# Kernel tuning notes

Hardware: AMD Instinct MI355X
Metric: run time of the kernel (lower is better)

## Reference

```python
import jax, jax.numpy as jnp
import numpy as np

IN_CHANNELS = 512
NUM_HEADS = 8
PARTIAL = 4
PC = IN_CHANNELS // PARTIAL  # 128, per-branch dim


def _mha(x, wqkv, bqkv, wproj, bproj, num_heads):
    # Standard ViT-style attention block: fused qkv -> SDPA -> out proj.
    B, N, C = x.shape
    d = C // num_heads
    qkv = (x @ wqkv + bqkv).reshape(B, N, 3, num_heads, d)
    q, k, v = jnp.moveaxis(qkv, 2, 0)            # each (B, N, h, d)
    q = q.transpose(0, 2, 1, 3)                  # (B, h, N, d)
    k = k.transpose(0, 2, 1, 3)
    v = v.transpose(0, 2, 1, 3)
    scale = jnp.asarray(d, x.dtype) ** -0.5
    attn = jax.nn.softmax(jnp.einsum('bhqd,bhkd->bhqk', q, k) * scale, axis=-1)
    out = jnp.einsum('bhqk,bhkd->bhqd', attn, v)
    out = out.transpose(0, 2, 1, 3).reshape(B, N, C)
    return out @ wproj + bproj


def _channel_shuffle(x, groups):
    # ShuffleNet channel shuffle on (b, c, n, t)
    b, c, n, t = x.shape
    return x.reshape(b, groups, c // groups, n, t).transpose(0, 2, 1, 3, 4).reshape(b, c, n, t)


def setup_inputs() -> dict:
    key = jax.random.key(0)
    ks = jax.random.split(key, 13)
    b, n, t = 8, 25, 64
    inp = {'x': jax.random.normal(ks[0], (b, n, t, IN_CHANNELS), dtype=jnp.float32)}
    i = 1
    for name in ('t', 's', 'st'):
        inp[f'{name}_wqkv'] = jax.random.normal(ks[i], (PC, 3 * PC), dtype=jnp.float32) * 0.02; i += 1
        inp[f'{name}_bqkv'] = jnp.zeros((3 * PC,), dtype=jnp.float32)
        inp[f'{name}_wproj'] = jax.random.normal(ks[i], (PC, PC), dtype=jnp.float32) * 0.02; i += 1
        inp[f'{name}_bproj'] = jnp.zeros((PC,), dtype=jnp.float32)
    return inp


def reference(x, t_wqkv, t_bqkv, t_wproj, t_bproj,
              s_wqkv, s_bqkv, s_wproj, s_bproj,
              st_wqkv, st_bqkv, st_wproj, st_bproj):
    b, n, t, c = x.shape
    pc = PC
    # split order in forward: x_id, x_st, x_s, x_t (all width pc here)
    x_id = x[..., 0 * pc:1 * pc]
    x_st = x[..., 1 * pc:2 * pc]
    x_s = x[..., 2 * pc:3 * pc]
    x_t = x[..., 3 * pc:4 * pc]

    t_x = x_t.reshape(b * n, t, pc)                       # temporal: attend over t
    s_x = x_s.transpose(0, 2, 1, 3).reshape(b * t, n, pc)  # spatial: attend over n
    st_x = x_st.reshape(b, n * t, pc)                      # spatiotemporal: attend over n*t

    t_x = _mha(t_x, t_wqkv, t_bqkv, t_wproj, t_bproj, NUM_HEADS).reshape(b, n, t, pc)
    s_x = _mha(s_x, s_wqkv, s_bqkv, s_wproj, s_bproj, NUM_HEADS).reshape(b, t, n, pc).transpose(0, 2, 1, 3)
    st_x = _mha(st_x, st_wqkv, st_bqkv, st_wproj, st_bproj, NUM_HEADS).reshape(b, n, t, pc)

    # concat order: id, t, s, st (differs from split order), then to channels-first
    out = jnp.concatenate((x_id, t_x, s_x, st_x), axis=3).transpose(0, 3, 1, 2)  # (b, c, n, t)
    return _channel_shuffle(out, PARTIAL)
```

## Files before the change

kernel.cpp:

```cpp
#include <hip/hip_runtime.h>
#include <hip/hip_bf16.h>

#define BUF   1638400ull
#define QSC   0.36067376f

typedef __attribute__((ext_vector_type(4))) float f4;
typedef __attribute__((ext_vector_type(8))) short s8v;
typedef __attribute__((ext_vector_type(4))) unsigned u4v;

#if __has_builtin(__builtin_amdgcn_exp2f)
#define EXP2(x) __builtin_amdgcn_exp2f(x)
#else
#define EXP2(x) exp2f(x)
#endif

__device__ __forceinline__ short f2bf(float f) {
    __hip_bfloat16 h = __float2bfloat16(f);
    short s; __builtin_memcpy(&s, &h, 2); return s;
}
__device__ __forceinline__ unsigned pack2(float a, float b) {
    return (unsigned)(unsigned short)f2bf(a) | ((unsigned)(unsigned short)f2bf(b) << 16);
}
__device__ __forceinline__ float bf2f(short s) {
    return __uint_as_float((unsigned)(unsigned short)s << 16);
}
__device__ __forceinline__ unsigned tpack(float hi, float lo) {
    return __builtin_amdgcn_perm(__float_as_uint(hi), __float_as_uint(lo), 0x07060302u);
}

__global__ __launch_bounds__(256) void prep(
    const float* __restrict__ x,
    const float* __restrict__ wq0, const float* __restrict__ wq1,
    const float* __restrict__ wq2,
    const float* __restrict__ wp0, const float* __restrict__ wp1,
    const float* __restrict__ wp2,
    short* __restrict__ xbf, short* __restrict__ wsw)
{
    const int blk = blockIdx.x, tid = threadIdx.x;
    if (blk < 3200) {
        const int base = blk * 2048 + tid * 8;
        float4 a = *(const float4*)(x + base);
        float4 b = *(const float4*)(x + base + 4);
        s8v o;
        o[0]=f2bf(a.x); o[1]=f2bf(a.y); o[2]=f2bf(a.z); o[3]=f2bf(a.w);
        o[4]=f2bf(b.x); o[5]=f2bf(b.y); o[6]=f2bf(b.z); o[7]=f2bf(b.w);
        *(s8v*)(xbf + base) = o;
    } else {
        const int idx0 = (blk - 3200) * 2048 + tid * 8;
        const float* W; int Ncols, loc = idx0;
        if      (idx0 < 49152)  { W = wq0; Ncols = 384; }
        else if (idx0 < 98304)  { W = wq1; Ncols = 384; loc -= 49152; }
        else if (idx0 < 147456) { W = wq2; Ncols = 384; loc -= 98304; }
        else if (idx0 < 163840) { W = wp0; Ncols = 128; loc -= 147456; }
        else if (idx0 < 180224) { W = wp1; Ncols = 128; loc -= 163840; }
        else                    { W = wp2; Ncols = 128; loc -= 180224; }
        const int lane = (loc >> 3) & 63, ks = (loc >> 9) & 3, nt = loc >> 11;
        const int col = nt * 16 + (lane & 15);
        const int k0  = ks * 32 + 8 * (lane >> 4);
        s8v o;
#pragma unroll
        for (int j = 0; j < 8; j++) o[j] = f2bf(W[(k0 + j) * Ncols + col]);
        *(s8v*)(wsw + idx0) = o;
    }
}

__global__ __launch_bounds__(256) void qkv_all(
    const short* __restrict__ xbf, const short* __restrict__ wsw,
    const float* __restrict__ bq0, const float* __restrict__ bq1,
    const float* __restrict__ bq2,
    short* __restrict__ q0, short* __restrict__ k0, short* __restrict__ vt0,
    short* __restrict__ q1, short* __restrict__ k1, short* __restrict__ vt1,
    short* __restrict__ q2, short* __restrict__ k2, short* __restrict__ vt2)
{
    const int br = blockIdx.x / 800, tile = blockIdx.x % 800;
    const int tok0 = tile * 16;
    const int wave = threadIdx.x >> 6, lane = threadIdx.x & 63;
    const int c = lane & 15, gq = lane >> 4;
    const int off = 384 - 128 * br;
    const short* wswb = wsw + br * 49152;
    const float* bias = (br == 0) ? bq0 : (br == 1) ? bq1 : bq2;

    const short* xrow = xbf + (size_t)(tok0 + c) * 512 + off + 8 * gq;
    s8v af[4];
#pragma unroll
    for (int ks = 0; ks < 4; ks++) af[ks] = *(const s8v*)(xrow + ks * 32);

    const int batch0 = tok0 >> 6;
    const int b_  = tok0 / 1600;
    const int rm0 = tok0 - b_ * 1600;
    const int seq1 = rm0 >> 6;

    for (int nti = 0; nti < 6; nti++) {
        const int nt = wave * 6 + nti;
        const short* bp = wswb + ((size_t)(nt * 4) * 64 + lane) * 8;
        f4 acc = {0.f, 0.f, 0.f, 0.f};
#pragma unroll
        for (int ks = 0; ks < 4; ks++) {
            s8v bf = *(const s8v*)(bp + ks * 512);
            acc = __builtin_amdgcn_mfma_f32_16x16x32_bf16(af[ks], bf, acc, 0, 0, 0);
        }
        const float bv = bias[nt * 16 + c];
        const float v0 = acc[0]+bv, v1 = acc[1]+bv, v2 = acc[2]+bv, v3 = acc[3]+bv;
        const int which = nt >> 3, h = nt & 7;

        if (br == 0) {
            const int seq0 = (tok0 & 63) + 4 * gq;
            if (which == 2) {
                unsigned* p = (unsigned*)(vt0 + ((size_t)(batch0*8+h)*16 + c)*64 + seq0);
                p[0] = pack2(v0, v1); p[1] = pack2(v2, v3);
            } else {
                short* p = (which ? k0 : q0) + (((size_t)(batch0*8+h)*64 + seq0)*16 + c);
                p[0]=f2bf(v0); p[16]=f2bf(v1); p[32]=f2bf(v2); p[48]=f2bf(v3);
            }
        } else if (br == 1) {
            const int bt0 = b_ * 64 + (rm0 & 63) + 4 * gq;
            if (which == 2) {
                short* p = vt1 + ((size_t)(bt0*8+h)*16 + c)*25 + seq1;
                p[0]=f2bf(v0); p[3200]=f2bf(v1); p[6400]=f2bf(v2); p[9600]=f2bf(v3);
            } else {
                short* p = (which ? k1 : q1) + (((size_t)bt0*8+h)*25 + seq1)*16 + c;
                p[0]=f2bf(v0); p[3200]=f2bf(v1); p[6400]=f2bf(v2); p[9600]=f2bf(v3);
            }
        } else {
            const int seq0 = rm0 + 4 * gq;
            if (which == 2) {
                unsigned* p = (unsigned*)(vt2 + ((size_t)b_*128 + h*16 + c)*1600 + seq0);
                p[0] = pack2(v0, v1); p[1] = pack2(v2, v3);
            } else {
                short* p = (which ? k2 : q2) + (((size_t)b_*8+h)*1600 + seq0)*16 + c;
                p[0]=f2bf(v0); p[16]=f2bf(v1); p[32]=f2bf(v2); p[48]=f2bf(v3);
            }
        }
    }
}

template<int CHK, int NCH, bool KM>
__device__ __forceinline__ void attn_core(
    const short* __restrict__ qg, const short* __restrict__ kg,
    const short* __restrict__ vtg, const int vstride, const int nreal,
    short* kl, short* vt, const int stid, const int snum,
    const int lane, const int qt0, const int nq,
    float* __restrict__ obase, const int ostride)
{
    const int c = lane & 15, gq = lane >> 4;
    const int VS = CHK + 8;

    u4v qu = {0u, 0u, 0u, 0u};
    if (gq < 2) {
        const int qrow = KM ? min(qt0 + c, nq - 1) : (qt0 + c);
        const short* qr = qg + (size_t)qrow * 16 + 8 * gq;
        s8v raw = *(const s8v*)qr;
#pragma unroll
        for (int jp = 0; jp < 4; jp++)
            qu[jp] = tpack(bf2f(raw[2*jp+1]) * QSC, bf2f(raw[2*jp]) * QSC);
    }
    const s8v qf = __builtin_bit_cast(s8v, qu);

    s8v ones;
#pragma unroll
    for (int j = 0; j < 8; j++) ones[j] = (short)0x3F80;

    f4 oacc = {0.f,0.f,0.f,0.f}, lacc = {0.f,0.f,0.f,0.f};
    const int krow_base = 8 * (c >> 2) + (c & 3);

    for (int ch = 0; ch < NCH; ch++) {
        const int kb0 = ch * CHK;
        __syncthreads();
        if (KM) {
            for (int i = stid; i < CHK * 16 + 8; i += snum)
                kl[i] = (i < nreal * 16) ? kg[i] : (short)0;
            for (int i = stid; i < 16 * VS; i += snum) {
                int d = i / VS, col = i % VS;
                vt[i] = (col < nreal) ? vtg[(size_t)d * vstride + col] : (short)0;
            }
        } else {
            const unsigned* kgd = (const unsigned*)(kg + (size_t)kb0 * 16);
            unsigned* kld = (unsigned*)kl;
            for (int i = stid; i < CHK * 8 + 4; i += snum)
                kld[i] = (i < CHK * 8) ? kgd[i] : 0u;
            for (int i = stid; i < 16 * (CHK / 2); i += snum) {
                int d = i / (CHK / 2), cc = i % (CHK / 2);
                *(unsigned*)(vt + d * VS + 2 * cc) =
                    *(const unsigned*)(vtg + (size_t)d * vstride + kb0 + 2 * cc);
            }
        }
        __syncthreads();

#pragma unroll
        for (int st = 0; st < CHK / 32; st++) {
            const int kr0 = st * 32 + krow_base;
            s8v kf0 = *(const s8v*)(gq < 2 ? kl + kr0 * 16 + 8 * gq       : kl + CHK * 16);
            s8v kf1 = *(const s8v*)(gq < 2 ? kl + (kr0 + 4) * 16 + 8 * gq : kl + CHK * 16);
            s8v vf  = *(const s8v*)(vt + c * VS + st * 32 + 8 * gq);

            const f4 z = {0.f,0.f,0.f,0.f};
            f4 sa = __builtin_amdgcn_mfma_f32_16x16x32_bf16(kf0, qf, z, 0, 0, 0);
            f4 sb = __builtin_amdgcn_mfma_f32_16x16x32_bf16(kf1, qf, z, 0, 0, 0);

            float pa[4], pb[4];
#pragma unroll
            for (int r = 0; r < 4; r++) { pa[r] = EXP2(sa[r]); pb[r] = EXP2(sb[r]); }
            if (KM) {
#pragma unroll
                for (int r = 0; r < 4; r++) {
                    if (kb0 + st*32 + 8*gq + r     >= nreal) pa[r] = 0.f;
                    if (kb0 + st*32 + 8*gq + 4 + r >= nreal) pb[r] = 0.f;
                }
            }
            u4v pu;
            pu[0] = tpack(pa[1], pa[0]); pu[1] = tpack(pa[3], pa[2]);
            pu[2] = tpack(pb[1], pb[0]); pu[3] = tpack(pb[3], pb[2]);
            s8v pf = __builtin_bit_cast(s8v, pu);

            oacc = __builtin_amdgcn_mfma_f32_16x16x32_bf16(pf, vf,   oacc, 0, 0, 0);
            lacc = __builtin_amdgcn_mfma_f32_16x16x32_bf16(pf, ones, lacc, 0, 0, 0);
        }
    }

#pragma unroll
    for (int r = 0; r < 4; r++) {
        const int qrow = qt0 + 4 * gq + r;
        if (!KM || qrow < nq)
            obase[(size_t)qrow * ostride] = oacc[r] / lacc[r];
    }
}

__global__ __launch_bounds__(256) void attn_all(
    const short* __restrict__ q0, const short* __restrict__ k0, const short* __restrict__ vt0,
    const short* __restrict__ q1, const short* __restrict__ k1, const short* __restrict__ vt1,
    const short* __restrict__ q2, const short* __restrict__ k2, const short* __restrict__ vt2,
    float* __restrict__ ob0, float* __restrict__ ob1, float* __restrict__ ob2)
{
    __shared__ short smem[5264];
    const int blk = blockIdx.x, tid = threadIdx.x;
    const int wave = tid >> 6, lane = tid & 63;
    const int c = lane & 15;

    if (blk < 1600) {
        const int bh = blk / 25, b25 = blk % 25;
        const int qt0 = b25 * 64 + wave * 16;
        float* obase = ob2 + (size_t)(bh >> 3) * 1600 * 128 + (bh & 7) * 16 + c;
        attn_core<160, 10, false>(q2 + (size_t)bh * 25600, k2 + (size_t)bh * 25600,
                                  vt2 + (size_t)bh * 25600, 1600, 1600,
                                  smem, smem + 2568, tid, 256,
                                  lane, qt0, 1600, obase, 128);
    } else if (blk < 3200) {
        const int bh = blk - 1600;
        float* obase = ob0 + (size_t)(bh >> 3) * 64 * 128 + (bh & 7) * 16 + c;
        attn_core<64, 1, false>(q0 + (size_t)bh * 1024, k0 + (size_t)bh * 1024,
                                vt0 + (size_t)bh * 1024, 64, 64,
                                smem, smem + 1040, tid, 256,
                                lane, wave * 16, 64, obase, 128);
    } else {
        const int bs = blk - 3200;
        const int half = wave >> 1;
        const int bh = bs * 2 + half;
        const int qt0 = (wave & 1) * 16;
        short* kl = smem + half * 1160;
        const int bat = bh >> 3, h = bh & 7;
        const int b2 = bat >> 6, t2 = bat & 63;
        float* obase = ob1 + ((size_t)b2 * 1600 + t2) * 128 + h * 16 + c;
        attn_core<32, 1, true>(q1 + (size_t)bh * 400, k1 + (size_t)bh * 400,
                               vt1 + (size_t)bh * 400, 25, 25,
                               kl, kl + 520, tid & 127, 128,
                               lane, qt0, 25, obase, 8192);
    }
}

__global__ __launch_bounds__(256) void projid(
    const float* __restrict__ ob0, const float* __restrict__ ob1,
    const float* __restrict__ ob2, const short* __restrict__ wsw,
    const float* __restrict__ bp0, const float* __restrict__ bp1,
    const float* __restrict__ bp2,
    const float* __restrict__ x, float* __restrict__ out)
{
    __shared__ unsigned short xl[64 * 130];
    const int blk = blockIdx.x, tid = threadIdx.x;

    if (blk < 2400) {
        const int br = blk / 800, t8 = blk % 800;
        const float* obb = (br == 0) ? ob0 : (br == 1) ? ob1 : ob2;
        const float* bp  = (br == 0) ? bp0 : (br == 1) ? bp1 : bp2;
        const short* wswb = wsw + 147456 + br * 16384;
        const int grp = br + 1;
        const int tok0 = t8 * 16;
        const int wave = tid >> 6, lane = tid & 63;
        const int c = lane & 15, gq = lane >> 4;

        const float* arow = obb + (size_t)(tok0 + c) * 128 + 8 * gq;
        s8v af[4];
#pragma unroll
        for (int ks = 0; ks < 4; ks++) {
            float4 a = *(const float4*)(arow + ks * 32);
            float4 b = *(const float4*)(arow + ks * 32 + 4);
            af[ks][0]=f2bf(a.x); af[ks][1]=f2bf(a.y); af[ks][2]=f2bf(a.z); af[ks][3]=f2bf(a.w);
            af[ks][4]=f2bf(b.x); af[ks][5]=f2bf(b.y); af[ks][6]=f2bf(b.z); af[ks][7]=f2bf(b.w);
        }

        const int bn = t8 >> 2, b_ = bn / 25, n_ = bn % 25;
        const int t0 = (t8 & 3) * 16 + 4 * gq;

        for (int nti = 0; nti < 2; nti++) {
            const int nt = wave * 2 + nti;
            const short* bpw = wswb + ((size_t)(nt * 4) * 64 + lane) * 8;
            f4 acc = {0.f, 0.f, 0.f, 0.f};
#pragma unroll
            for (int ks = 0; ks < 4; ks++) {
                s8v bf = *(const s8v*)(bpw + ks * 512);
                acc = __builtin_amdgcn_mfma_f32_16x16x32_bf16(af[ks], bf, acc, 0, 0, 0);
            }
            const int c2 = nt * 16 + c;
            const float bv = bp[c2];
            float4 st = {acc[0]+bv, acc[1]+bv, acc[2]+bv, acc[3]+bv};
            *(float4*)(out + (size_t)b_ * 819200 + (size_t)(c2 * 4 + grp) * 1600
                           + n_ * 64 + t0) = st;
        }
    } else {
        const int bn = blk - 2400;
        const int b_ = bn / 25, n_ = bn % 25;
        for (int idx = tid; idx < 8192; idx += 256) {
            int row = idx >> 7, c2 = idx & 127;
            xl[row * 130 + c2] =
                (unsigned short)(__float_as_uint(x[(size_t)(bn * 64 + row) * 512 + c2]) >> 16);
        }
        __syncthreads();
        const int t_ = tid & 63, cg = tid >> 6;
        const size_t base = (size_t)b_ * 819200 + (size_t)n_ * 64 + t_;
#pragma unroll
        for (int i = 0; i < 32; i++) {
            int c2 = cg + 4 * i;
            out[base + (size_t)(c2 * 4 + 0) * 1600] =
                __uint_as_float((unsigned)xl[t_ * 130 + c2] << 16);
        }
    }
}

extern "C" void kernel_launch(void* const* d_in, const int* in_sizes, int n_in,
                              void* d_out, int out_size, void* d_ws, size_t ws_size,
                              hipStream_t stream)
{
    const float* x        = (const float*)d_in[0];
    const float* t_wqkv   = (const float*)d_in[1];
    const float* t_bqkv   = (const float*)d_in[2];
    const float* t_wproj  = (const float*)d_in[3];
    const float* t_bproj  = (const float*)d_in[4];
    const float* s_wqkv   = (const float*)d_in[5];
    const float* s_bqkv   = (const float*)d_in[6];
    const float* s_wproj  = (const float*)d_in[7];
    const float* s_bproj  = (const float*)d_in[8];
    const float* st_wqkv  = (const float*)d_in[9];
    const float* st_bqkv  = (const float*)d_in[10];
    const float* st_wproj = (const float*)d_in[11];
    const float* st_bproj = (const float*)d_in[12];

    short* xbf = (short*)d_ws;
    short* wsw = xbf + 6553600ull;
    short* qkv = wsw + 196608ull;
    short *q0 = qkv,           *k0 = qkv + BUF,     *vt0 = qkv + 2*BUF;
    short *q1 = qkv + 3*BUF,   *k1 = qkv + 4*BUF,   *vt1 = qkv + 5*BUF;
    short *q2 = qkv + 6*BUF,   *k2 = qkv + 7*BUF,   *vt2 = qkv + 8*BUF;
    float* ob0 = (float*)(qkv + 9*BUF);
    float* ob1 = ob0 + BUF;
    float* ob2 = ob0 + 2*BUF;
    float* out = (float*)d_out;

    prep<<<3296, 256, 0, stream>>>(x, t_wqkv, s_wqkv, st_wqkv,
                                   t_wproj, s_wproj, st_wproj, xbf, wsw);
    qkv_all<<<2400, 256, 0, stream>>>(xbf, wsw, t_bqkv, s_bqkv, st_bqkv,
                                      q0, k0, vt0, q1, k1, vt1, q2, k2, vt2);
    attn_all<<<5248, 256, 0, stream>>>(q0, k0, vt0, q1, k1, vt1, q2, k2, vt2,
                                       ob0, ob1, ob2);
    projid<<<2600, 256, 0, stream>>>(ob0, ob1, ob2, wsw,
                                     t_bproj, s_bproj, st_bproj, x, out);
}
```

Before: 189.1 us.

## Fuse temporal and spatial attention branches into single kernels keeping QKV in LDS

Splits the work by branch. The temporal and spatial branches each get one fused kernel that computes QKV, attention and the output projection with intermediates kept in shared memory, so their q/k/v and fp32 attention outputs no longer round-trip through global memory. The spatiotemporal branch keeps separate qkv, attention and projection kernels, but its attention output is now stored as bf16 instead of fp32. In exchange there are more kernel launches, and the fused kernels launch few blocks (200 and 512), which risks poor occupancy and serialization across the CUs.

```diff
diff --git a/kernel.cpp b/kernel.cpp
--- a/kernel.cpp
+++ b/kernel.cpp
@@ -26,6 +26,12 @@
 }
 __device__ __forceinline__ unsigned tpack(float hi, float lo) {
     return __builtin_amdgcn_perm(__float_as_uint(hi), __float_as_uint(lo), 0x07060302u);
+}
+__device__ __forceinline__ s8v ones_frag() {
+    s8v o;
+#pragma unroll
+    for (int j = 0; j < 8; j++) o[j] = (short)0x3F80;
+    return o;
 }
 
 __global__ __launch_bounds__(256) void prep(
@@ -64,31 +70,22 @@
     }
 }
 
-__global__ __launch_bounds__(256) void qkv_all(
+__global__ __launch_bounds__(256) void qkv_st(
     const short* __restrict__ xbf, const short* __restrict__ wsw,
-    const float* __restrict__ bq0, const float* __restrict__ bq1,
-    const float* __restrict__ bq2,
-    short* __restrict__ q0, short* __restrict__ k0, short* __restrict__ vt0,
-    short* __restrict__ q1, short* __restrict__ k1, short* __restrict__ vt1,
+    const float* __restrict__ bias,
     short* __restrict__ q2, short* __restrict__ k2, short* __restrict__ vt2)
 {
-    const int br = blockIdx.x / 800, tile = blockIdx.x % 800;
-    const int tok0 = tile * 16;
+    const int tok0 = blockIdx.x * 16;
     const int wave = threadIdx.x >> 6, lane = threadIdx.x & 63;
     const int c = lane & 15, gq = lane >> 4;
-    const int off = 384 - 128 * br;
-    const short* wswb = wsw + br * 49152;
-    const float* bias = (br == 0) ? bq0 : (br == 1) ? bq1 : bq2;
-
-    const short* xrow = xbf + (size_t)(tok0 + c) * 512 + off + 8 * gq;
+    const short* wswb = wsw + 98304;
+    const short* xrow = xbf + (size_t)(tok0 + c) * 512 + 128 + 8 * gq;
     s8v af[4];
 #pragma unroll
     for (int ks = 0; ks < 4; ks++) af[ks] = *(const s8v*)(xrow + ks * 32);
 
-    const int batch0 = tok0 >> 6;
     const int b_  = tok0 / 1600;
     const int rm0 = tok0 - b_ * 1600;
-    const int seq1 = rm0 >> 6;
 
     for (int nti = 0; nti < 6; nti++) {
         const int nt = wave * 6 + nti;
@@ -102,95 +99,69 @@
         const float bv = bias[nt * 16 + c];
         const float v0 = acc[0]+bv, v1 = acc[1]+bv, v2 = acc[2]+bv, v3 = acc[3]+bv;
         const int which = nt >> 3, h = nt & 7;
-
-        if (br == 0) {
-            const int seq0 = (tok0 & 63) + 4 * gq;
-            if (which == 2) {
-                unsigned* p = (unsigned*)(vt0 + ((size_t)(batch0*8+h)*16 + c)*64 + seq0);
-                p[0] = pack2(v0, v1); p[1] = pack2(v2, v3);
-            } else {
-                short* p = (which ? k0 : q0) + (((size_t)(batch0*8+h)*64 + seq0)*16 + c);
-                p[0]=f2bf(v0); p[16]=f2bf(v1); p[32]=f2bf(v2); p[48]=f2bf(v3);
-            }
-        } else if (br == 1) {
-            const int bt0 = b_ * 64 + (rm0 & 63) + 4 * gq;
-            if (which == 2) {
-                short* p = vt1 + ((size_t)(bt0*8+h)*16 + c)*25 + seq1;
-                p[0]=f2bf(v0); p[3200]=f2bf(v1); p[6400]=f2bf(v2); p[9600]=f2bf(v3);
-            } else {
-                short* p = (which ? k1 : q1) + (((size_t)bt0*8+h)*25 + seq1)*16 + c;
-                p[0]=f2bf(v0); p[3200]=f2bf(v1); p[6400]=f2bf(v2); p[9600]=f2bf(v3);
-            }
+        const int seq0 = rm0 + 4 * gq;
+        if (which == 2) {
+            unsigned* p = (unsigned*)(vt2 + ((size_t)b_*128 + h*16 + c)*1600 + seq0);
+            p[0] = pack2(v0, v1); p[1] = pack2(v2, v3);
         } else {
-            const int seq0 = rm0 + 4 * gq;
-            if (which == 2) {
-                unsigned* p = (unsigned*)(vt2 + ((size_t)b_*128 + h*16 + c)*1600 + seq0);
-                p[0] = pack2(v0, v1); p[1] = pack2(v2, v3);
-            } else {
-                short* p = (which ? k2 : q2) + (((size_t)b_*8+h)*1600 + seq0)*16 + c;
-                p[0]=f2bf(v0); p[16]=f2bf(v1); p[32]=f2bf(v2); p[48]=f2bf(v3);
-            }
-        }
-    }
-}
-
-template<int CHK, int NCH, bool KM>
-__device__ __forceinline__ void attn_core(
-    const short* __restrict__ qg, const short* __restrict__ kg,
-    const short* __restrict__ vtg, const int vstride, const int nreal,
-    short* kl, short* vt, const int stid, const int snum,
-    const int lane, const int qt0, const int nq,
-    float* __restrict__ obase, const int ostride)
-{
+            short* p = (which ? k2 : q2) + (((size_t)b_*8+h)*1600 + seq0)*16 + c;
+            p[0]=f2bf(v0); p[16]=f2bf(v1); p[32]=f2bf(v2); p[48]=f2bf(v3);
+        }
+    }
+}
+
+#define CH 160
+#define VS (CH + 8)
+
+__global__ __launch_bounds__(256) void attn_st(
+    const short* __restrict__ q2, const short* __restrict__ k2,
+    const short* __restrict__ vt2, short* __restrict__ ob2)
+{
+    __shared__ short kl[CH * 16 + 8];
+    __shared__ short vt[16 * VS];
+
+    const int bh = blockIdx.x / 25, b25 = blockIdx.x % 25;
+    const int tid = threadIdx.x;
+    const int wave = tid >> 6, lane = tid & 63;
     const int c = lane & 15, gq = lane >> 4;
-    const int VS = CHK + 8;
+    const int qt0 = b25 * 64 + wave * 16;
+
+    const short* qg  = q2  + (size_t)bh * 25600;
+    const short* kg  = k2  + (size_t)bh * 25600;
+    const short* vtg = vt2 + (size_t)bh * 25600;
 
     u4v qu = {0u, 0u, 0u, 0u};
     if (gq < 2) {
-        const int qrow = KM ? min(qt0 + c, nq - 1) : (qt0 + c);
-        const short* qr = qg + (size_t)qrow * 16 + 8 * gq;
-        s8v raw = *(const s8v*)qr;
+        s8v raw = *(const s8v*)(qg + (size_t)(qt0 + c) * 16 + 8 * gq);
 #pragma unroll
         for (int jp = 0; jp < 4; jp++)
             qu[jp] = tpack(bf2f(raw[2*jp+1]) * QSC, bf2f(raw[2*jp]) * QSC);
     }
     const s8v qf = __builtin_bit_cast(s8v, qu);
-
-    s8v ones;
-#pragma unroll
-    for (int j = 0; j < 8; j++) ones[j] = (short)0x3F80;
+    const s8v ones = ones_frag();
 
     f4 oacc = {0.f,0.f,0.f,0.f}, lacc = {0.f,0.f,0.f,0.f};
     const int krow_base = 8 * (c >> 2) + (c & 3);
 
-    for (int ch = 0; ch < NCH; ch++) {
-        const int kb0 = ch * CHK;
+    for (int ch = 0; ch < 10; ch++) {
+        const int kb0 = ch * CH;
         __syncthreads();
-        if (KM) {
-            for (int i = stid; i < CHK * 16 + 8; i += snum)
-                kl[i] = (i < nreal * 16) ? kg[i] : (short)0;
-            for (int i = stid; i < 16 * VS; i += snum) {
-                int d = i / VS, col = i % VS;
-                vt[i] = (col < nreal) ? vtg[(size_t)d * vstride + col] : (short)0;
-            }
-        } else {
-            const unsigned* kgd = (const unsigned*)(kg + (size_t)kb0 * 16);
-            unsigned* kld = (unsigned*)kl;
-            for (int i = stid; i < CHK * 8 + 4; i += snum)
-                kld[i] = (i < CHK * 8) ? kgd[i] : 0u;
-            for (int i = stid; i < 16 * (CHK / 2); i += snum) {
-                int d = i / (CHK / 2), cc = i % (CHK / 2);
-                *(unsigned*)(vt + d * VS + 2 * cc) =
-                    *(const unsigned*)(vtg + (size_t)d * vstride + kb0 + 2 * cc);
-            }
+        const unsigned* kgd = (const unsigned*)(kg + (size_t)kb0 * 16);
+        unsigned* kld = (unsigned*)kl;
+        for (int i = tid; i < CH * 8 + 4; i += 256)
+            kld[i] = (i < CH * 8) ? kgd[i] : 0u;
+        for (int i = tid; i < 16 * (CH / 2); i += 256) {
+            int d = i / (CH / 2), cc = i % (CH / 2);
+            *(unsigned*)(vt + d * VS + 2 * cc) =
+                *(const unsigned*)(vtg + (size_t)d * 1600 + kb0 + 2 * cc);
         }
         __syncthreads();
 
 #pragma unroll
-        for (int st = 0; st < CHK / 32; st++) {
+        for (int st = 0; st < 5; st++) {
             const int kr0 = st * 32 + krow_base;
-            s8v kf0 = *(const s8v*)(gq < 2 ? kl + kr0 * 16 + 8 * gq       : kl + CHK * 16);
-            s8v kf1 = *(const s8v*)(gq < 2 ? kl + (kr0 + 4) * 16 + 8 * gq : kl + CHK * 16);
+            s8v kf0 = *(const s8v*)(gq < 2 ? kl + kr0 * 16 + 8 * gq       : kl + CH * 16);
+            s8v kf1 = *(const s8v*)(gq < 2 ? kl + (kr0 + 4) * 16 + 8 * gq : kl + CH * 16);
             s8v vf  = *(const s8v*)(vt + c * VS + st * 32 + 8 * gq);
 
             const f4 z = {0.f,0.f,0.f,0.f};
@@ -200,13 +171,6 @@
             float pa[4], pb[4];
 #pragma unroll
             for (int r = 0; r < 4; r++) { pa[r] = EXP2(sa[r]); pb[r] = EXP2(sb[r]); }
-            if (KM) {
-#pragma unroll
-                for (int r = 0; r < 4; r++) {
-                    if (kb0 + st*32 + 8*gq + r     >= nreal) pa[r] = 0.f;
-                    if (kb0 + st*32 + 8*gq + 4 + r >= nreal) pb[r] = 0.f;
-                }
-            }
             u4v pu;
             pu[0] = tpack(pa[1], pa[0]); pu[1] = tpack(pa[3], pa[2]);
             pu[2] = tpack(pb[1], pb[0]); pu[3] = tpack(pb[3], pb[2]);
@@ -217,106 +181,280 @@
         }
     }
 
+    const int batch = bh >> 3, h = bh & 7;
 #pragma unroll
     for (int r = 0; r < 4; r++) {
         const int qrow = qt0 + 4 * gq + r;
-        if (!KM || qrow < nq)
-            obase[(size_t)qrow * ostride] = oacc[r] / lacc[r];
-    }
-}
-
-__global__ __launch_bounds__(256) void attn_all(
-    const short* __restrict__ q0, const short* __restrict__ k0, const short* __restrict__ vt0,
-    const short* __restrict__ q1, const short* __restrict__ k1, const short* __restrict__ vt1,
-    const short* __restrict__ q2, const short* __restrict__ k2, const short* __restrict__ vt2,
-    float* __restrict__ ob0, float* __restrict__ ob1, float* __restrict__ ob2)
-{
-    __shared__ short smem[5264];
-    const int blk = blockIdx.x, tid = threadIdx.x;
-    const int wave = tid >> 6, lane = tid & 63;
-    const int c = lane & 15;
-
-    if (blk < 1600) {
-        const int bh = blk / 25, b25 = blk % 25;
-        const int qt0 = b25 * 64 + wave * 16;
-        float* obase = ob2 + (size_t)(bh >> 3) * 1600 * 128 + (bh & 7) * 16 + c;
-        attn_core<160, 10, false>(q2 + (size_t)bh * 25600, k2 + (size_t)bh * 25600,
-                                  vt2 + (size_t)bh * 25600, 1600, 1600,
-                                  smem, smem + 2568, tid, 256,
-                                  lane, qt0, 1600, obase, 128);
-    } else if (blk < 3200) {
-        const int bh = blk - 1600;
-        float* obase = ob0 + (size_t)(bh >> 3) * 64 * 128 + (bh & 7) * 16 + c;
-        attn_core<64, 1, false>(q0 + (size_t)bh * 1024, k0 + (size_t)bh * 1024,
-                                vt0 + (size_t)bh * 1024, 64, 64,
-                                smem, smem + 1040, tid, 256,
-                                lane, wave * 16, 64, obase, 128);
-    } else {
-        const int bs = blk - 3200;
-        const int half = wave >> 1;
-        const int bh = bs * 2 + half;
-        const int qt0 = (wave & 1) * 16;
-        short* kl = smem + half * 1160;
-        const int bat = bh >> 3, h = bh & 7;
-        const int b2 = bat >> 6, t2 = bat & 63;
-        float* obase = ob1 + ((size_t)b2 * 1600 + t2) * 128 + h * 16 + c;
-        attn_core<32, 1, true>(q1 + (size_t)bh * 400, k1 + (size_t)bh * 400,
-                               vt1 + (size_t)bh * 400, 25, 25,
-                               kl, kl + 520, tid & 127, 128,
-                               lane, qt0, 25, obase, 8192);
-    }
-}
-
-__global__ __launch_bounds__(256) void projid(
-    const float* __restrict__ ob0, const float* __restrict__ ob1,
-    const float* __restrict__ ob2, const short* __restrict__ wsw,
-    const float* __restrict__ bp0, const float* __restrict__ bp1,
-    const float* __restrict__ bp2,
-    const float* __restrict__ x, float* __restrict__ out)
-{
-    __shared__ unsigned short xl[64 * 130];
-    const int blk = blockIdx.x, tid = threadIdx.x;
-
-    if (blk < 2400) {
-        const int br = blk / 800, t8 = blk % 800;
-        const float* obb = (br == 0) ? ob0 : (br == 1) ? ob1 : ob2;
-        const float* bp  = (br == 0) ? bp0 : (br == 1) ? bp1 : bp2;
-        const short* wswb = wsw + 147456 + br * 16384;
-        const int grp = br + 1;
-        const int tok0 = t8 * 16;
-        const int wave = tid >> 6, lane = tid & 63;
-        const int c = lane & 15, gq = lane >> 4;
-
-        const float* arow = obb + (size_t)(tok0 + c) * 128 + 8 * gq;
+        ob2[((size_t)batch * 1600 + qrow) * 128 + h * 16 + c] =
+            f2bf(oacc[r] / lacc[r]);
+    }
+}
+
+__global__ __launch_bounds__(256) void t_fused(
+    const short* __restrict__ xbf, const short* __restrict__ wsw,
+    const float* __restrict__ bq, const float* __restrict__ bp,
+    float* __restrict__ out)
+{
+    __shared__ short ql[8 * 64 * 20];
+    __shared__ short kl[8 * 64 * 20];
+    __shared__ short vtl[8 * 16 * 68];
+    __shared__ short obl[64 * 132];
+
+    const int bn = blockIdx.x;
+    const int wave = threadIdx.x >> 6, lane = threadIdx.x & 63;
+    const int c = lane & 15, gq = lane >> 4;
+
+    {
+        const short* xrow = xbf + (size_t)(bn * 64 + wave * 16 + c) * 512 + 384 + 8 * gq;
         s8v af[4];
 #pragma unroll
-        for (int ks = 0; ks < 4; ks++) {
-            float4 a = *(const float4*)(arow + ks * 32);
-            float4 b = *(const float4*)(arow + ks * 32 + 4);
-            af[ks][0]=f2bf(a.x); af[ks][1]=f2bf(a.y); af[ks][2]=f2bf(a.z); af[ks][3]=f2bf(a.w);
-            af[ks][4]=f2bf(b.x); af[ks][5]=f2bf(b.y); af[ks][6]=f2bf(b.z); af[ks][7]=f2bf(b.w);
-        }
-
-        const int bn = t8 >> 2, b_ = bn / 25, n_ = bn % 25;
-        const int t0 = (t8 & 3) * 16 + 4 * gq;
-
-        for (int nti = 0; nti < 2; nti++) {
-            const int nt = wave * 2 + nti;
-            const short* bpw = wswb + ((size_t)(nt * 4) * 64 + lane) * 8;
+        for (int ks = 0; ks < 4; ks++) af[ks] = *(const s8v*)(xrow + ks * 32);
+        const int seq0 = wave * 16 + 4 * gq;
+        for (int nt = 0; nt < 24; nt++) {
+            const short* bpw = wsw + ((size_t)(nt * 4) * 64 + lane) * 8;
             f4 acc = {0.f, 0.f, 0.f, 0.f};
 #pragma unroll
             for (int ks = 0; ks < 4; ks++) {
                 s8v bf = *(const s8v*)(bpw + ks * 512);
                 acc = __builtin_amdgcn_mfma_f32_16x16x32_bf16(af[ks], bf, acc, 0, 0, 0);
             }
+            const float bv = bq[nt * 16 + c];
+            const float v0 = acc[0]+bv, v1 = acc[1]+bv, v2 = acc[2]+bv, v3 = acc[3]+bv;
+            const int which = nt >> 3, h = nt & 7;
+            if (which == 2) {
+                unsigned* p = (unsigned*)&vtl[(h * 16 + c) * 68 + seq0];
+                p[0] = pack2(v0, v1); p[1] = pack2(v2, v3);
+            } else {
+                short* p = (which ? kl : ql) + (h * 64 + seq0) * 20 + c;
+                p[0]=f2bf(v0); p[20]=f2bf(v1); p[40]=f2bf(v2); p[60]=f2bf(v3);
+            }
+        }
+    }
+    __syncthreads();
+
+    {
+        const s8v ones = ones_frag();
+        const int krow_base = 8 * (c >> 2) + (c & 3);
+        for (int j = 0; j < 8; j++) {
+            const int h = wave * 2 + (j >> 2), qt = j & 3;
+            u4v qu = {0u, 0u, 0u, 0u};
+            if (gq < 2) {
+                s8v raw = *(const s8v*)&ql[(h * 64 + qt * 16 + c) * 20 + 8 * gq];
+#pragma unroll
+                for (int jp = 0; jp < 4; jp++)
+                    qu[jp] = tpack(bf2f(raw[2*jp+1]) * QSC, bf2f(raw[2*jp]) * QSC);
+            }
+            const s8v qf = __builtin_bit_cast(s8v, qu);
+            f4 oacc = {0.f,0.f,0.f,0.f}, lacc = {0.f,0.f,0.f,0.f};
+#pragma unroll
+            for (int st = 0; st < 2; st++) {
+                const int kr0 = st * 32 + krow_base;
+                s8v kf0 = *(const s8v*)&kl[(h * 64 + kr0)     * 20 + 8 * (gq & 1)];
+                s8v kf1 = *(const s8v*)&kl[(h * 64 + kr0 + 4) * 20 + 8 * (gq & 1)];
+                s8v vf  = *(const s8v*)&vtl[(h * 16 + c) * 68 + st * 32 + 8 * gq];
+                const f4 z = {0.f,0.f,0.f,0.f};
+                f4 sa = __builtin_amdgcn_mfma_f32_16x16x32_bf16(kf0, qf, z, 0, 0, 0);
+                f4 sb = __builtin_amdgcn_mfma_f32_16x16x32_bf16(kf1, qf, z, 0, 0, 0);
+                float pa[4], pb[4];
+#pragma unroll
+                for (int r = 0; r < 4; r++) { pa[r] = EXP2(sa[r]); pb[r] = EXP2(sb[r]); }
+                u4v pu;
+                pu[0] = tpack(pa[1], pa[0]); pu[1] = tpack(pa[3], pa[2]);
+                pu[2] = tpack(pb[1], pb[0]); pu[3] = tpack(pb[3], pb[2]);
+                s8v pf = __builtin_bit_cast(s8v, pu);
+                oacc = __builtin_amdgcn_mfma_f32_16x16x32_bf16(pf, vf,   oacc, 0, 0, 0);
+                lacc = __builtin_amdgcn_mfma_f32_16x16x32_bf16(pf, ones, lacc, 0, 0, 0);
+            }
+#pragma unroll
+            for (int r = 0; r < 4; r++)
+                obl[(qt * 16 + 4 * gq + r) * 132 + h * 16 + c] = f2bf(oacc[r] / lacc[r]);
+        }
+    }
+    __syncthreads();
+
+    {
+        const short* wswp = wsw + 147456;
+        s8v ap[4];
+#pragma unroll
+        for (int ks = 0; ks < 4; ks++)
+            ap[ks] = *(const s8v*)&obl[(wave * 16 + c) * 132 + ks * 32 + 8 * gq];
+        const int b_ = bn / 25, n_ = bn % 25;
+        const int t0 = wave * 16 + 4 * gq;
+        for (int nt = 0; nt < 8; nt++) {
+            const short* bpw = wswp + ((size_t)(nt * 4) * 64 + lane) * 8;
+            f4 acc = {0.f, 0.f, 0.f, 0.f};
+#pragma unroll
+            for (int ks = 0; ks < 4; ks++) {
+                s8v bf = *(const s8v*)(bpw + ks * 512);
+                acc = __builtin_amdgcn_mfma_f32_16x16x32_bf16(ap[ks], bf, acc, 0, 0, 0);
+            }
             const int c2 = nt * 16 + c;
             const float bv = bp[c2];
             float4 st = {acc[0]+bv, acc[1]+bv, acc[2]+bv, acc[3]+bv};
-            *(float4*)(out + (size_t)b_ * 819200 + (size_t)(c2 * 4 + grp) * 1600
+            *(float4*)(out + (size_t)b_ * 819200 + (size_t)(c2 * 4 + 1) * 1600
                            + n_ * 64 + t0) = st;
         }
+    }
+}
+
+__global__ __launch_bounds__(256) void s_fused(
+    const short* __restrict__ xbf, const short* __restrict__ wsw,
+    const float* __restrict__ bq, const float* __restrict__ bp,
+    float* __restrict__ out)
+{
+    __shared__ short ql[8 * 32 * 20];
+    __shared__ short kl[8 * 32 * 20];
+    __shared__ short vtl[8 * 16 * 34];
+    __shared__ short obl[32 * 132];
+
+    const int bt = blockIdx.x;
+    const int b_ = bt >> 6, t_ = bt & 63;
+    const int wave = threadIdx.x >> 6, lane = threadIdx.x & 63;
+    const int c = lane & 15, gq = lane >> 4;
+
+    {
+        const int mt = wave & 1;
+        const int nrow = min(mt * 16 + c, 24);
+        const short* xrow = xbf + ((size_t)b_ * 1600 + nrow * 64 + t_) * 512 + 256 + 8 * gq;
+        s8v af[4];
+#pragma unroll
+        for (int ks = 0; ks < 4; ks++) af[ks] = *(const s8v*)(xrow + ks * 32);
+        const int seq0 = mt * 16 + 4 * gq;
+        const short* wswq = wsw + 49152;
+        for (int jj = 0; jj < 12; jj++) {
+            const int nt = (wave >> 1) * 12 + jj;
+            const short* bpw = wswq + ((size_t)(nt * 4) * 64 + lane) * 8;
+            f4 acc = {0.f, 0.f, 0.f, 0.f};
+#pragma unroll
+            for (int ks = 0; ks < 4; ks++) {
+                s8v bf = *(const s8v*)(bpw + ks * 512);
+                acc = __builtin_amdgcn_mfma_f32_16x16x32_bf16(af[ks], bf, acc, 0, 0, 0);
+            }
+            const float bv = bq[nt * 16 + c];
+            const float v0 = acc[0]+bv, v1 = acc[1]+bv, v2 = acc[2]+bv, v3 = acc[3]+bv;
+            const int which = nt >> 3, h = nt & 7;
+            if (which == 2) {
+                unsigned* p = (unsigned*)&vtl[(h * 16 + c) * 34 + seq0];
+                p[0] = pack2(v0, v1); p[1] = pack2(v2, v3);
+            } else {
+                short* p = (which ? kl : ql) + (h * 32 + seq0) * 20 + c;
+                p[0]=f2bf(v0); p[20]=f2bf(v1); p[40]=f2bf(v2); p[60]=f2bf(v3);
+            }
+        }
+    }
+    __syncthreads();
+
+    {
+        const s8v ones = ones_frag();
+        const int krow_base = 8 * (c >> 2) + (c & 3);
+        for (int j = 0; j < 4; j++) {
+            const int h = wave * 2 + (j >> 1), qt = j & 1;
+            u4v qu = {0u, 0u, 0u, 0u};
+            if (gq < 2) {
+                s8v raw = *(const s8v*)&ql[(h * 32 + qt * 16 + c) * 20 + 8 * gq];
+#pragma unroll
+                for (int jp = 0; jp < 4; jp++)
+                    qu[jp] = tpack(bf2f(raw[2*jp+1]) * QSC, bf2f(raw[2*jp]) * QSC);
+            }
+            const s8v qf = __builtin_bit_cast(s8v, qu);
+            s8v kf0 = *(const s8v*)&kl[(h * 32 + krow_base)     * 20 + 8 * (gq & 1)];
+            s8v kf1 = *(const s8v*)&kl[(h * 32 + krow_base + 4) * 20 + 8 * (gq & 1)];
+            s8v vf  = *(const s8v*)&vtl[(h * 16 + c) * 34 + 8 * gq];
+            const f4 z = {0.f,0.f,0.f,0.f};
+            f4 sa = __builtin_amdgcn_mfma_f32_16x16x32_bf16(kf0, qf, z, 0, 0, 0);
+            f4 sb = __builtin_amdgcn_mfma_f32_16x16x32_bf16(kf1, qf, z, 0, 0, 0);
+            float pa[4], pb[4];
+#pragma unroll
+            for (int r = 0; r < 4; r++) {
+                pa[r] = (8 * gq + r     < 25) ? EXP2(sa[r]) : 0.f;
+                pb[r] = (8 * gq + 4 + r < 25) ? EXP2(sb[r]) : 0.f;
+            }
+            u4v pu;
+            pu[0] = tpack(pa[1], pa[0]); pu[1] = tpack(pa[3], pa[2]);
+            pu[2] = tpack(pb[1], pb[0]); pu[3] = tpack(pb[3], pb[2]);
+            s8v pf = __builtin_bit_cast(s8v, pu);
+            f4 oacc = {0.f,0.f,0.f,0.f}, lacc = {0.f,0.f,0.f,0.f};
+            oacc = __builtin_amdgcn_mfma_f32_16x16x32_bf16(pf, vf,   oacc, 0, 0, 0);
+            lacc = __builtin_amdgcn_mfma_f32_16x16x32_bf16(pf, ones, lacc, 0, 0, 0);
+#pragma unroll
+            for (int r = 0; r < 4; r++) {
+                const int qrow = qt * 16 + 4 * gq + r;
+                if (qrow < 25)
+                    obl[qrow * 132 + h * 16 + c] = f2bf(oacc[r] / lacc[r]);
+            }
+        }
+    }
+    __syncthreads();
+
+    {
+        const short* wswp = wsw + 163840;
+        const int mt = wave & 1;
+        const int arow = min(mt * 16 + c, 24);
+        s8v ap[4];
+#pragma unroll
+        for (int ks = 0; ks < 4; ks++)
+            ap[ks] = *(const s8v*)&obl[arow * 132 + ks * 32 + 8 * gq];
+        for (int jj = 0; jj < 4; jj++) {
+            const int nt = (wave >> 1) * 4 + jj;
+            const short* bpw = wswp + ((size_t)(nt * 4) * 64 + lane) * 8;
+            f4 acc = {0.f, 0.f, 0.f, 0.f};
+#pragma unroll
+            for (int ks = 0; ks < 4; ks++) {
+                s8v bf = *(const s8v*)(bpw + ks * 512);
+                acc = __builtin_amdgcn_mfma_f32_16x16x32_bf16(ap[ks], bf, acc, 0, 0, 0);
+            }
+            const int c2 = nt * 16 + c;
+            const float bv = bp[c2];
+#pragma unroll
+            for (int r = 0; r < 4; r++) {
+                const int n = mt * 16 + 4 * gq + r;
+                if (n < 25)
+                    out[(size_t)b_ * 819200 + (size_t)(c2 * 4 + 2) * 1600
+                        + n * 64 + t_] = acc[r] + bv;
+            }
+        }
+    }
+}
+
+__global__ __launch_bounds__(256) void projst_id(
+    const short* __restrict__ ob2, const short* __restrict__ wsw,
+    const float* __restrict__ bp, const float* __restrict__ x,
+    float* __restrict__ out)
+{
+    __shared__ unsigned short xl[64 * 130];
+    const int blk = blockIdx.x, tid = threadIdx.x;
+
+    if (blk < 800) {
+        const int tok0 = blk * 16;
+        const int wave = tid >> 6, lane = tid & 63;
+        const int c = lane & 15, gq = lane >> 4;
+        const short* wswp = wsw + 180224;
+
+        s8v af[4];
+#pragma unroll
+        for (int ks = 0; ks < 4; ks++)
+            af[ks] = *(const s8v*)(ob2 + (size_t)(tok0 + c) * 128 + ks * 32 + 8 * gq);
+
+        const int bn = blk >> 2, b_ = bn / 25, n_ = bn % 25;
+        const int t0 = (blk & 3) * 16 + 4 * gq;
+
+        for (int nti = 0; nti < 2; nti++) {
+            const int nt = wave * 2 + nti;
+            const short* bpw = wswp + ((size_t)(nt * 4) * 64 + lane) * 8;
+            f4 acc = {0.f, 0.f, 0.f, 0.f};
+#pragma unroll
+            for (int ks = 0; ks < 4; ks++) {
+                s8v bf = *(const s8v*)(bpw + ks * 512);
+                acc = __builtin_amdgcn_mfma_f32_16x16x32_bf16(af[ks], bf, acc, 0, 0, 0);
+            }
+            const int c2 = nt * 16 + c;
+            const float bv = bp[c2];
+            float4 st = {acc[0]+bv, acc[1]+bv, acc[2]+bv, acc[3]+bv};
+            *(float4*)(out + (size_t)b_ * 819200 + (size_t)(c2 * 4 + 3) * 1600
+                           + n_ * 64 + t0) = st;
+        }
     } else {
-        const int bn = blk - 2400;
+        const int bn = blk - 800;
         const int b_ = bn / 25, n_ = bn % 25;
         for (int idx = tid; idx < 8192; idx += 256) {
             int row = idx >> 7, c2 = idx & 127;
@@ -355,21 +493,17 @@
 
     short* xbf = (short*)d_ws;
     short* wsw = xbf + 6553600ull;
-    short* qkv = wsw + 196608ull;
-    short *q0 = qkv,           *k0 = qkv + BUF,     *vt0 = qkv + 2*BUF;
-    short *q1 = qkv + 3*BUF,   *k1 = qkv + 4*BUF,   *vt1 = qkv + 5*BUF;
-    short *q2 = qkv + 6*BUF,   *k2 = qkv + 7*BUF,   *vt2 = qkv + 8*BUF;
-    float* ob0 = (float*)(qkv + 9*BUF);
-    float* ob1 = ob0 + BUF;
-    float* ob2 = ob0 + 2*BUF;
+    short* q2  = wsw + 196608ull;
+    short* k2  = q2 + BUF;
+    short* vt2 = q2 + 2 * BUF;
+    short* ob2 = q2 + 3 * BUF;
     float* out = (float*)d_out;
 
     prep<<<3296, 256, 0, stream>>>(x, t_wqkv, s_wqkv, st_wqkv,
                                    t_wproj, s_wproj, st_wproj, xbf, wsw);
-    qkv_all<<<2400, 256, 0, stream>>>(xbf, wsw, t_bqkv, s_bqkv, st_bqkv,
-                                      q0, k0, vt0, q1, k1, vt1, q2, k2, vt2);
-    attn_all<<<5248, 256, 0, stream>>>(q0, k0, vt0, q1, k1, vt1, q2, k2, vt2,
-                                       ob0, ob1, ob2);
-    projid<<<2600, 256, 0, stream>>>(ob0, ob1, ob2, wsw,
-                                     t_bproj, s_bproj, st_bproj, x, out);
-}
+    qkv_st<<<800, 256, 0, stream>>>(xbf, wsw, st_bqkv, q2, k2, vt2);
+    t_fused<<<200, 256, 0, stream>>>(xbf, wsw, t_bqkv, t_bproj, out);
+    s_fused<<<512, 256, 0, stream>>>(xbf, wsw, s_bqkv, s_bproj, out);
+    attn_st<<<1600, 256, 0, stream>>>(q2, k2, vt2, ob2);
+    projst_id<<<1000, 256, 0, stream>>>(ob2, wsw, st_bproj, x, out);
+}
```

New measurement: 201.9 us. +6.7%, slower.
